# Optimization experiments

Measured on AMD Instinct MI355X. Metric: run time of the kernel, lower is better.

## Reference

```python
import jax, jax.numpy as jnp
import numpy as np

N = 129      # num_of_nodes hardcoded in EvolveGCNH(129, in_channels)
IN = 129     # in_channels; must satisfy ceil(IN/129 * N) == IN for GRU shapes
OUT = 64     # out_channels of final linear
E = 4096     # number of edges (avg degree ~32)


def setup_inputs() -> dict:
    key = jax.random.key(0)
    ks = jax.random.split(key, 12)
    s = 1.0 / np.sqrt(IN)
    x = jax.random.normal(ks[0], (N, IN), jnp.float32)
    edge_index = jax.random.randint(ks[1], (2, E), 0, N)
    edge_weight = jax.random.uniform(ks[2], (E,), jnp.float32, minval=0.1, maxval=1.0)
    # TopKPooling projection vector p
    pool_p = jax.random.normal(ks[3], (IN,), jnp.float32) * s
    # initial GCN weight (GRU hidden state), glorot-ish
    W0 = jax.random.normal(ks[4], (IN, IN), jnp.float32) * s
    # GRU parameters (torch layout: rows ordered [reset; update; new])
    w_ih = jax.random.normal(ks[5], (3 * IN, IN), jnp.float32) * s
    w_hh = jax.random.normal(ks[6], (3 * IN, IN), jnp.float32) * s
    b_ih = jax.random.normal(ks[7], (3 * IN,), jnp.float32) * s
    b_hh = jax.random.normal(ks[8], (3 * IN,), jnp.float32) * s
    conv_bias = jax.random.normal(ks[9], (IN,), jnp.float32) * s
    lin_w = jax.random.normal(ks[10], (OUT, IN), jnp.float32) * s
    lin_b = jax.random.normal(ks[11], (OUT,), jnp.float32) * s
    return {"x": x, "edge_index": edge_index, "edge_weight": edge_weight,
            "pool_p": pool_p, "W0": W0, "w_ih": w_ih, "w_hh": w_hh,
            "b_ih": b_ih, "b_hh": b_hh, "conv_bias": conv_bias,
            "lin_w": lin_w, "lin_b": lin_b}


def reference(x, edge_index, edge_weight, pool_p, W0, w_ih, w_hh, b_ih, b_hh,
              conv_bias, lin_w, lin_b):
    n = x.shape[0]
    # F.dropout in eval mode (training=False) -> identity.

    # --- TopKPooling: score = tanh(x @ p / ||p||); select top-k (k == IN == N) ---
    score = jnp.tanh((x @ pool_p) / jnp.linalg.norm(pool_p))
    perm = jnp.argsort(-score)                     # descending, k = IN = n
    x_tilde = x[perm] * score[perm][:, None]       # [k, IN]

    # --- GRU step: input batch = k pooled nodes, hidden = evolving weight W0 [IN, IN] ---
    gi = x_tilde @ w_ih.T + b_ih                   # [k, 3*IN]
    gh = W0 @ w_hh.T + b_hh                        # [IN, 3*IN]
    ir, iz, i_n = jnp.split(gi, 3, axis=1)
    hr, hz, h_n = jnp.split(gh, 3, axis=1)
    r = jax.nn.sigmoid(ir + hr)
    z = jax.nn.sigmoid(iz + hz)
    cand = jnp.tanh(i_n + r * h_n)
    W = (1.0 - z) * cand + z * W0                  # evolved GCN weight [IN, IN]

    # --- GCNConv_Fixed_W: gcn_norm with self-loops, then D^-1/2 A D^-1/2 (x @ W) ---
    row, col = edge_index[0], edge_index[1]        # source, target
    loop = jnp.arange(n)
    row_f = jnp.concatenate([row, loop])
    col_f = jnp.concatenate([col, loop])
    ew_f = jnp.concatenate([edge_weight, jnp.ones((n,), x.dtype)])
    deg = jax.ops.segment_sum(ew_f, col_f, num_segments=n)
    dis = jnp.where(deg > 0, jax.lax.rsqrt(jnp.maximum(deg, 1e-12)), 0.0)
    norm = dis[row_f] * ew_f * dis[col_f]          # [E+n]
    xw = x @ W                                     # [N, IN]
    out = jax.ops.segment_sum(norm[:, None] * xw[row_f], col_f, num_segments=n)
    out = out + conv_bias

    # --- ELU + Linear ---
    h = jax.nn.elu(out)
    return h @ lin_w.T + lin_b
```

## Files before the change

kernel.cpp:

```cpp
#include <hip/hip_runtime.h>
#include <math.h>

#define NN 129
#define INC 129
#define OUTC 64
#define NE 4096
#define WCAP 32

__device__ __forceinline__ float sigmf(float x) { return 1.0f / (1.0f + expf(-x)); }

__global__ __launch_bounds__(1024) void k_prep(
    const float* __restrict__ x, const float* __restrict__ p,
    const int* __restrict__ col, const float* __restrict__ ew,
    float* __restrict__ score, int* __restrict__ perm, float* __restrict__ dis)
{
    int b = blockIdx.x, t = threadIdx.x;
    int wv = t >> 6, lane = t & 63;

    if (b == 0) {
        __shared__ float ssc[NN];
        __shared__ float s_rinv;
        if (wv == 0) {
            float a = 0.f;
            for (int c = lane; c < INC; c += 64) { float pv = p[c]; a += pv * pv; }
            for (int o = 32; o; o >>= 1) a += __shfl_xor(a, o, 64);
            if (lane == 0) s_rinv = 1.0f / sqrtf(a);
        }
        for (int n = wv; n < NN; n += 16) {
            const float* xr = x + (size_t)n * INC;
            float a = 0.f;
            for (int c = lane; c < INC; c += 64) a += xr[c] * p[c];
            for (int o = 32; o; o >>= 1) a += __shfl_xor(a, o, 64);
            if (lane == 0) ssc[n] = a;
        }
        __syncthreads();
        if (t < NN) { float sc = tanhf(ssc[t] * s_rinv); ssc[t] = sc; score[t] = sc; }
        __syncthreads();
        if (t < NN) {
            float my = ssc[t];
            int rank = 0;
            #pragma unroll 16
            for (int j = 0; j < NN; ++j) {
                float o = ssc[j];
                rank += (o > my || (o == my && j < t)) ? 1 : 0;
            }
            perm[rank] = t;
        }
    } else {
        __shared__ float red[16];
        int n = b - 1;
        float d = 0.f;
        for (int e = t; e < NE; e += 1024) d += (col[e] == n) ? ew[e] : 0.f;
        for (int o = 32; o; o >>= 1) d += __shfl_xor(d, o, 64);
        if (lane == 0) red[wv] = d;
        __syncthreads();
        if (t == 0) {
            float s = 1.0f;
            for (int w = 0; w < 16; ++w) s += red[w];
            dis[n] = rsqrtf(fmaxf(s, 1e-12f));
        }
    }
}

__global__ __launch_bounds__(256) void k_gru(
    const float* __restrict__ x, const float* __restrict__ score,
    const int* __restrict__ perm, const float* __restrict__ W0,
    const float* __restrict__ w_ih, const float* __restrict__ w_hh,
    const float* __restrict__ b_ih, const float* __restrict__ b_hh,
    float* __restrict__ W)
{
    int lane = threadIdx.x & 63;
    int wid = blockIdx.x * 4 + (threadIdx.x >> 6);
    if (wid >= NN * INC) return;
    int i = wid / INC;
    int j = wid - i * INC;
    int pi = perm[i];
    float sc = score[pi];
    const float* xr = x  + (size_t)pi * INC;
    const float* h0 = W0 + (size_t)i * INC;
    const float* wr = w_ih + (size_t)j * INC;
    const float* wz = wr + (size_t)INC * INC;
    const float* wn = wz + (size_t)INC * INC;
    const float* vr = w_hh + (size_t)j * INC;
    const float* vz = vr + (size_t)INC * INC;
    const float* vn = vz + (size_t)INC * INC;

    float sr = 0.f, szv = 0.f, an = 0.f, hn = 0.f;
    for (int c = lane; c < INC; c += 64) {
        float xv = xr[c] * sc;
        float hv = h0[c];
        sr  += xv * wr[c] + hv * vr[c];
        szv += xv * wz[c] + hv * vz[c];
        an  += xv * wn[c];
        hn  += hv * vn[c];
    }
    for (int o = 32; o; o >>= 1) {
        sr  += __shfl_xor(sr,  o, 64);
        szv += __shfl_xor(szv, o, 64);
        an  += __shfl_xor(an,  o, 64);
        hn  += __shfl_xor(hn,  o, 64);
    }
    if (lane == 0) {
        float r    = sigmf(sr  + b_ih[j]           + b_hh[j]);
        float z    = sigmf(szv + b_ih[INC + j]     + b_hh[INC + j]);
        float cand = tanhf(an + b_ih[2 * INC + j] + r * (hn + b_hh[2 * INC + j]));
        W[(size_t)i * INC + j] = (1.0f - z) * cand + z * h0[j];
    }
}

__global__ __launch_bounds__(1024) void k_fin(
    const float* __restrict__ x, const int* __restrict__ ei,
    const float* __restrict__ ew, const float* __restrict__ dis,
    const float* __restrict__ W, const float* __restrict__ cb,
    const float* __restrict__ lw, const float* __restrict__ lb,
    float* __restrict__ out)
{
    __shared__ float s_dis[NN];
    __shared__ int   s_r[16 * WCAP];
    __shared__ float s_w[16 * WCAP];
    __shared__ int   s_cnt[16];
    __shared__ int   s_off[17];
    __shared__ int   s_dr[16 * WCAP];
    __shared__ float s_nrm[16 * WCAP];
    __shared__ float s_a[NN];
    __shared__ float s_h[NN];
    int c = blockIdx.x, t = threadIdx.x;
    int wv = t >> 6, lane = t & 63;
    const int* row = ei;
    const int* col = ei + NE;

    if (t < NN) s_dis[t] = dis[t];

    int base = wv * 256;
    int cnt = 0;
    #pragma unroll
    for (int it = 0; it < 4; ++it) {
        int e = base + it * 64 + lane;
        int rr = row[e];
        float wval = ew[e];
        bool m = (col[e] == c);
        unsigned long long mask = __ballot(m);
        if (m) {
            int pos = cnt + __popcll(mask & ((1ull << lane) - 1));
            if (pos < WCAP) { s_r[wv * WCAP + pos] = rr; s_w[wv * WCAP + pos] = wval; }
        }
        cnt += __popcll(mask);
    }
    if (lane == 0) s_cnt[wv] = min(cnt, WCAP);
    __syncthreads();

    if (t == 0) {
        int acc = 0;
        for (int w = 0; w < 16; ++w) { s_off[w] = acc; acc += s_cnt[w]; }
        s_off[16] = acc;
    }
    __syncthreads();

    float dc = s_dis[c];
    {
        int wc = s_cnt[wv];
        if (lane < wc) {
            int r = s_r[wv * WCAP + lane];
            s_dr[s_off[wv] + lane]  = r;
            s_nrm[s_off[wv] + lane] = s_dis[r] * s_w[wv * WCAP + lane] * dc;
        }
    }
    __syncthreads();

    int tot = s_off[16];
    if (t < NN) {
        float a = dc * dc * x[(size_t)c * INC + t];
        #pragma unroll 8
        for (int k = 0; k < tot; ++k)
            a += s_nrm[k] * x[(size_t)s_dr[k] * INC + t];
        s_a[t] = a;
    }
    __syncthreads();

    if (t < NN) {
        float g = cb[t];
        #pragma unroll 16
        for (int cc = 0; cc < NN; ++cc) g += s_a[cc] * W[(size_t)cc * INC + t];
        s_h[t] = (g > 0.f) ? g : expm1f(g);
    }
    __syncthreads();

    for (int f = wv; f < OUTC; f += 16) {
        const float* wrow = lw + (size_t)f * INC;
        float a = 0.f;
        for (int cc = lane; cc < INC; cc += 64) a += s_h[cc] * wrow[cc];
        for (int o = 32; o; o >>= 1) a += __shfl_xor(a, o, 64);
        if (lane == 0) out[(size_t)c * OUTC + f] = a + lb[f];
    }
}

extern "C" void kernel_launch(void* const* d_in, const int* in_sizes, int n_in,
                              void* d_out, int out_size, void* d_ws, size_t ws_size,
                              hipStream_t stream)
{
    const float* x   = (const float*)d_in[0];
    const int*   ei  = (const int*)d_in[1];
    const float* ew  = (const float*)d_in[2];
    const float* pp  = (const float*)d_in[3];
    const float* W0  = (const float*)d_in[4];
    const float* wih = (const float*)d_in[5];
    const float* whh = (const float*)d_in[6];
    const float* bih = (const float*)d_in[7];
    const float* bhh = (const float*)d_in[8];
    const float* cb  = (const float*)d_in[9];
    const float* lw  = (const float*)d_in[10];
    const float* lb  = (const float*)d_in[11];
    float* out = (float*)d_out;

    char* ws = (char*)d_ws;
    float* score = (float*)(ws + 0);
    int*   perm  = (int*)  (ws + 640);
    float* dis   = (float*)(ws + 1280);
    float* W     = (float*)(ws + 2048);

    const int* col = ei + NE;

    k_prep<<<NN + 1, 1024, 0, stream>>>(x, pp, col, ew, score, perm, dis);

    int gru_blocks = (NN * INC + 3) / 4;
    k_gru<<<gru_blocks, 256, 0, stream>>>(x, score, perm, W0, wih, whh, bih, bhh, W);

    k_fin<<<NN, 1024, 0, stream>>>(x, ei, ew, dis, W, cb, lw, lb, out);
}
```

Before: 35.78 us.

## Fuse top-k scoring, GRU, and graph aggregation into one kernel

Merges the prep and GRU kernels. Each GRU block now recomputes the pooling scores and the rank-sort permutation redundantly in shared memory and then handles two weight entries per wave. Extra blocks in the same launch compute degrees with shared atomics and the sparse neighbor aggregation A·x, writing it to a workspace. The final kernel then only does agg@W with a wave-split reduction plus ELU and the linear layer. This removes one launch and one dependency, at the cost of 521 blocks each repeating the score, norm and sort work.

```diff
diff --git a/kernel.cpp b/kernel.cpp
--- a/kernel.cpp
+++ b/kernel.cpp
@@ -5,20 +5,27 @@
 #define INC 129
 #define OUTC 64
 #define NE 4096
+#define NGRU 521
 #define WCAP 32
 
 __device__ __forceinline__ float sigmf(float x) { return 1.0f / (1.0f + expf(-x)); }
 
-__global__ __launch_bounds__(1024) void k_prep(
-    const float* __restrict__ x, const float* __restrict__ p,
-    const int* __restrict__ col, const float* __restrict__ ew,
-    float* __restrict__ score, int* __restrict__ perm, float* __restrict__ dis)
+__global__ __launch_bounds__(1024) void k_big(
+    const float* __restrict__ x, const int* __restrict__ ei,
+    const float* __restrict__ ew, const float* __restrict__ p,
+    const float* __restrict__ W0, const float* __restrict__ w_ih,
+    const float* __restrict__ w_hh, const float* __restrict__ b_ih,
+    const float* __restrict__ b_hh, float* __restrict__ W,
+    float* __restrict__ agg)
 {
     int b = blockIdx.x, t = threadIdx.x;
     int wv = t >> 6, lane = t & 63;
-
-    if (b == 0) {
-        __shared__ float ssc[NN];
+    const int* row = ei;
+    const int* col = ei + NE;
+
+    if (b < NGRU) {
+        __shared__ float s_sc[NN];
+        __shared__ int   s_perm[NN];
         __shared__ float s_rinv;
         if (wv == 0) {
             float a = 0.f;
@@ -31,158 +38,149 @@
             float a = 0.f;
             for (int c = lane; c < INC; c += 64) a += xr[c] * p[c];
             for (int o = 32; o; o >>= 1) a += __shfl_xor(a, o, 64);
-            if (lane == 0) ssc[n] = a;
-        }
-        __syncthreads();
-        if (t < NN) { float sc = tanhf(ssc[t] * s_rinv); ssc[t] = sc; score[t] = sc; }
+            if (lane == 0) s_sc[n] = a;
+        }
+        __syncthreads();
+        if (t < NN) s_sc[t] = tanhf(s_sc[t] * s_rinv);
         __syncthreads();
         if (t < NN) {
-            float my = ssc[t];
+            float my = s_sc[t];
             int rank = 0;
             #pragma unroll 16
             for (int j = 0; j < NN; ++j) {
-                float o = ssc[j];
+                float o = s_sc[j];
                 rank += (o > my || (o == my && j < t)) ? 1 : 0;
             }
-            perm[rank] = t;
+            s_perm[rank] = t;
+        }
+        __syncthreads();
+
+        int gw = b * 16 + wv;
+        #pragma unroll
+        for (int jj = 0; jj < 2; ++jj) {
+            int wid = gw * 2 + jj;
+            if (wid >= NN * INC) continue;
+            int i = wid / INC;
+            int j = wid - i * INC;
+            int pi = s_perm[i];
+            float sc = s_sc[pi];
+            const float* xr = x  + (size_t)pi * INC;
+            const float* h0 = W0 + (size_t)i * INC;
+            const float* wr = w_ih + (size_t)j * INC;
+            const float* wz = wr + (size_t)INC * INC;
+            const float* wn = wz + (size_t)INC * INC;
+            const float* vr = w_hh + (size_t)j * INC;
+            const float* vz = vr + (size_t)INC * INC;
+            const float* vn = vz + (size_t)INC * INC;
+
+            float sr = 0.f, szv = 0.f, an = 0.f, hn = 0.f;
+            for (int c = lane; c < INC; c += 64) {
+                float xv = xr[c] * sc;
+                float hv = h0[c];
+                sr  += xv * wr[c] + hv * vr[c];
+                szv += xv * wz[c] + hv * vz[c];
+                an  += xv * wn[c];
+                hn  += hv * vn[c];
+            }
+            for (int o = 32; o; o >>= 1) {
+                sr  += __shfl_xor(sr,  o, 64);
+                szv += __shfl_xor(szv, o, 64);
+                an  += __shfl_xor(an,  o, 64);
+                hn  += __shfl_xor(hn,  o, 64);
+            }
+            if (lane == 0) {
+                float r    = sigmf(sr  + b_ih[j]           + b_hh[j]);
+                float z    = sigmf(szv + b_ih[INC + j]     + b_hh[INC + j]);
+                float cand = tanhf(an + b_ih[2 * INC + j] + r * (hn + b_hh[2 * INC + j]));
+                W[(size_t)i * INC + j] = (1.0f - z) * cand + z * h0[j];
+            }
         }
     } else {
-        __shared__ float red[16];
-        int n = b - 1;
-        float d = 0.f;
-        for (int e = t; e < NE; e += 1024) d += (col[e] == n) ? ew[e] : 0.f;
-        for (int o = 32; o; o >>= 1) d += __shfl_xor(d, o, 64);
-        if (lane == 0) red[wv] = d;
+        int c = b - NGRU;
+        __shared__ float s_deg[NN];
+        __shared__ float s_dis[NN];
+        __shared__ int   s_r[16 * WCAP];
+        __shared__ float s_w[16 * WCAP];
+        __shared__ int   s_cnt[16];
+        __shared__ int   s_off[17];
+        __shared__ int   s_dr[16 * WCAP];
+        __shared__ float s_nrm[16 * WCAP];
+
+        if (t < NN) s_deg[t] = 0.f;
+        __syncthreads();
+        for (int e = t; e < NE; e += 1024) atomicAdd(&s_deg[col[e]], ew[e]);
+        __syncthreads();
+        if (t < NN) s_dis[t] = rsqrtf(fmaxf(s_deg[t] + 1.0f, 1e-12f));
+        __syncthreads();
+
+        int basee = wv * 256;
+        int cnt = 0;
+        #pragma unroll
+        for (int it = 0; it < 4; ++it) {
+            int e = basee + it * 64 + lane;
+            int rr = row[e];
+            float wval = ew[e];
+            bool m = (col[e] == c);
+            unsigned long long mask = __ballot(m);
+            if (m) {
+                int pos = cnt + __popcll(mask & ((1ull << lane) - 1));
+                if (pos < WCAP) { s_r[wv * WCAP + pos] = rr; s_w[wv * WCAP + pos] = wval; }
+            }
+            cnt += __popcll(mask);
+        }
+        if (lane == 0) s_cnt[wv] = min(cnt, WCAP);
         __syncthreads();
         if (t == 0) {
-            float s = 1.0f;
-            for (int w = 0; w < 16; ++w) s += red[w];
-            dis[n] = rsqrtf(fmaxf(s, 1e-12f));
+            int acc = 0;
+            for (int w = 0; w < 16; ++w) { s_off[w] = acc; acc += s_cnt[w]; }
+            s_off[16] = acc;
+        }
+        __syncthreads();
+        float dc = s_dis[c];
+        if (lane < s_cnt[wv]) {
+            int r = s_r[wv * WCAP + lane];
+            s_dr[s_off[wv] + lane]  = r;
+            s_nrm[s_off[wv] + lane] = s_dis[r] * s_w[wv * WCAP + lane] * dc;
+        }
+        __syncthreads();
+        int tot = s_off[16];
+        if (t < NN) {
+            float a = dc * dc * x[(size_t)c * INC + t];
+            #pragma unroll 8
+            for (int k = 0; k < tot; ++k)
+                a += s_nrm[k] * x[(size_t)s_dr[k] * INC + t];
+            agg[(size_t)c * INC + t] = a;
         }
     }
 }
 
-__global__ __launch_bounds__(256) void k_gru(
-    const float* __restrict__ x, const float* __restrict__ score,
-    const int* __restrict__ perm, const float* __restrict__ W0,
-    const float* __restrict__ w_ih, const float* __restrict__ w_hh,
-    const float* __restrict__ b_ih, const float* __restrict__ b_hh,
-    float* __restrict__ W)
+__global__ __launch_bounds__(1024) void k_fin(
+    const float* __restrict__ agg, const float* __restrict__ W,
+    const float* __restrict__ cb, const float* __restrict__ lw,
+    const float* __restrict__ lb, float* __restrict__ out)
 {
-    int lane = threadIdx.x & 63;
-    int wid = blockIdx.x * 4 + (threadIdx.x >> 6);
-    if (wid >= NN * INC) return;
-    int i = wid / INC;
-    int j = wid - i * INC;
-    int pi = perm[i];
-    float sc = score[pi];
-    const float* xr = x  + (size_t)pi * INC;
-    const float* h0 = W0 + (size_t)i * INC;
-    const float* wr = w_ih + (size_t)j * INC;
-    const float* wz = wr + (size_t)INC * INC;
-    const float* wn = wz + (size_t)INC * INC;
-    const float* vr = w_hh + (size_t)j * INC;
-    const float* vz = vr + (size_t)INC * INC;
-    const float* vn = vz + (size_t)INC * INC;
-
-    float sr = 0.f, szv = 0.f, an = 0.f, hn = 0.f;
-    for (int c = lane; c < INC; c += 64) {
-        float xv = xr[c] * sc;
-        float hv = h0[c];
-        sr  += xv * wr[c] + hv * vr[c];
-        szv += xv * wz[c] + hv * vz[c];
-        an  += xv * wn[c];
-        hn  += hv * vn[c];
-    }
-    for (int o = 32; o; o >>= 1) {
-        sr  += __shfl_xor(sr,  o, 64);
-        szv += __shfl_xor(szv, o, 64);
-        an  += __shfl_xor(an,  o, 64);
-        hn  += __shfl_xor(hn,  o, 64);
-    }
-    if (lane == 0) {
-        float r    = sigmf(sr  + b_ih[j]           + b_hh[j]);
-        float z    = sigmf(szv + b_ih[INC + j]     + b_hh[INC + j]);
-        float cand = tanhf(an + b_ih[2 * INC + j] + r * (hn + b_hh[2 * INC + j]));
-        W[(size_t)i * INC + j] = (1.0f - z) * cand + z * h0[j];
-    }
-}
-
-__global__ __launch_bounds__(1024) void k_fin(
-    const float* __restrict__ x, const int* __restrict__ ei,
-    const float* __restrict__ ew, const float* __restrict__ dis,
-    const float* __restrict__ W, const float* __restrict__ cb,
-    const float* __restrict__ lw, const float* __restrict__ lb,
-    float* __restrict__ out)
-{
-    __shared__ float s_dis[NN];
-    __shared__ int   s_r[16 * WCAP];
-    __shared__ float s_w[16 * WCAP];
-    __shared__ int   s_cnt[16];
-    __shared__ int   s_off[17];
-    __shared__ int   s_dr[16 * WCAP];
-    __shared__ float s_nrm[16 * WCAP];
     __shared__ float s_a[NN];
+    __shared__ float s_g[NN];
     __shared__ float s_h[NN];
     int c = blockIdx.x, t = threadIdx.x;
     int wv = t >> 6, lane = t & 63;
-    const int* row = ei;
-    const int* col = ei + NE;
-
-    if (t < NN) s_dis[t] = dis[t];
-
-    int base = wv * 256;
-    int cnt = 0;
-    #pragma unroll
-    for (int it = 0; it < 4; ++it) {
-        int e = base + it * 64 + lane;
-        int rr = row[e];
-        float wval = ew[e];
-        bool m = (col[e] == c);
-        unsigned long long mask = __ballot(m);
-        if (m) {
-            int pos = cnt + __popcll(mask & ((1ull << lane) - 1));
-            if (pos < WCAP) { s_r[wv * WCAP + pos] = rr; s_w[wv * WCAP + pos] = wval; }
-        }
-        cnt += __popcll(mask);
+
+    if (t < NN) { s_a[t] = agg[(size_t)c * INC + t]; s_g[t] = cb[t]; }
+    __syncthreads();
+
+    float p0 = 0.f, p1 = 0.f, p2 = 0.f;
+    for (int cc = wv; cc < NN; cc += 16) {
+        float av = s_a[cc];
+        const float* wr = W + (size_t)cc * INC;
+        p0 += av * wr[lane];
+        p1 += av * wr[lane + 64];
+        if (lane == 0) p2 += av * wr[128];
     }
-    if (lane == 0) s_cnt[wv] = min(cnt, WCAP);
+    atomicAdd(&s_g[lane], p0);
+    atomicAdd(&s_g[lane + 64], p1);
+    if (lane == 0) atomicAdd(&s_g[128], p2);
     __syncthreads();
-
-    if (t == 0) {
-        int acc = 0;
-        for (int w = 0; w < 16; ++w) { s_off[w] = acc; acc += s_cnt[w]; }
-        s_off[16] = acc;
-    }
-    __syncthreads();
-
-    float dc = s_dis[c];
-    {
-        int wc = s_cnt[wv];
-        if (lane < wc) {
-            int r = s_r[wv * WCAP + lane];
-            s_dr[s_off[wv] + lane]  = r;
-            s_nrm[s_off[wv] + lane] = s_dis[r] * s_w[wv * WCAP + lane] * dc;
-        }
-    }
-    __syncthreads();
-
-    int tot = s_off[16];
-    if (t < NN) {
-        float a = dc * dc * x[(size_t)c * INC + t];
-        #pragma unroll 8
-        for (int k = 0; k < tot; ++k)
-            a += s_nrm[k] * x[(size_t)s_dr[k] * INC + t];
-        s_a[t] = a;
-    }
-    __syncthreads();
-
-    if (t < NN) {
-        float g = cb[t];
-        #pragma unroll 16
-        for (int cc = 0; cc < NN; ++cc) g += s_a[cc] * W[(size_t)cc * INC + t];
-        s_h[t] = (g > 0.f) ? g : expm1f(g);
-    }
+    if (t < NN) { float g = s_g[t]; s_h[t] = (g > 0.f) ? g : expm1f(g); }
     __syncthreads();
 
     for (int f = wv; f < OUTC; f += 16) {
@@ -213,17 +211,11 @@
     float* out = (float*)d_out;
 
     char* ws = (char*)d_ws;
-    float* score = (float*)(ws + 0);
-    int*   perm  = (int*)  (ws + 640);
-    float* dis   = (float*)(ws + 1280);
-    float* W     = (float*)(ws + 2048);
-
-    const int* col = ei + NE;
-
-    k_prep<<<NN + 1, 1024, 0, stream>>>(x, pp, col, ew, score, perm, dis);
-
-    int gru_blocks = (NN * INC + 3) / 4;
-    k_gru<<<gru_blocks, 256, 0, stream>>>(x, score, perm, W0, wih, whh, bih, bhh, W);
-
-    k_fin<<<NN, 1024, 0, stream>>>(x, ei, ew, dis, W, cb, lw, lb, out);
+    float* W   = (float*)(ws + 0);
+    float* agg = (float*)(ws + 69632);
+
+    k_big<<<NGRU + NN, 1024, 0, stream>>>(
+        x, ei, ew, pp, W0, wih, whh, bih, bhh, W, agg);
+
+    k_fin<<<NN, 1024, 0, stream>>>(agg, W, cb, lw, lb, out);
 }
```

After: 54.87 us. 53.4% more time.
